# Kernel optimization log

Measured on AMD Instinct MI355X. Metric: run time of the kernel, lower is better.

## Reference

```python
import jax, jax.numpy as jnp
import numpy as np

N = 8192      # agent_num
F = 128       # feature dim
P = 16        # persona dim
E = 262144    # edges (N * avg_degree 32)


def setup_inputs() -> dict:
    key = jax.random.key(0)
    ks = jax.random.split(key, 10)
    return {
        "feature": jax.random.normal(ks[0], (N, F), dtype=jnp.float32),
        "next_feature": jax.random.normal(ks[1], (N, F), dtype=jnp.float32),
        "persona_t": jax.random.uniform(ks[2], (N, P), dtype=jnp.float32),
        "alpha": jax.random.normal(ks[3], (P,), dtype=jnp.float32),
        "beta": jax.random.normal(ks[4], (P,), dtype=jnp.float32),
        "gamma": jax.random.normal(ks[5], (P,), dtype=jnp.float32),
        "act_src": jax.random.randint(ks[6], (E,), 0, N, dtype=jnp.int32),
        "act_dst": jax.random.randint(ks[7], (E,), 0, N, dtype=jnp.int32),
        "edge_src": jax.random.randint(ks[8], (E,), 0, N, dtype=jnp.int32),
        "edge_dst": jax.random.randint(ks[9], (E,), 0, N, dtype=jnp.int32),
    }


def _row_l2_normalize(x):
    # norm_func: divide each row by its L2 norm (scatter-add of squares in torch)
    norms = jnp.sqrt(jnp.sum(x * x, axis=1, keepdims=True))
    return x / norms


def reference(feature, next_feature, persona_t, alpha, beta, gamma,
              act_src, act_dst, edge_src, edge_dst):
    n, f = feature.shape

    # ---- impact (gamma) path: adj_sim_self(next_action, old - new) ----
    diff = feature - next_feature                           # [N, F]
    # hadamard(adj, diff @ diff.T): only dot products on action edges
    impact_vals = jnp.sum(diff[act_src] * diff[act_dst], axis=1) / f   # [E]
    gamma_row = persona_t @ gamma                            # [N] persona-weighted gamma
    reward_impact = impact_vals * gamma_row[act_src]         # row-wise multiply

    # ---- similarity (alpha) path: adj_sim(next_action, norm(next_feature)) ----
    # step() normalizes next_feature, then adj_sim normalizes again (idempotent)
    nf = _row_l2_normalize(_row_l2_normalize(next_feature))  # [N, F]
    sim_vals = jnp.sum(nf[act_src] * nf[act_dst], axis=1)    # [E] cosine sims on edges
    alpha_row = persona_t @ alpha                            # [N]
    reward_sim = sim_vals * alpha_row[act_src]

    # ---- cost (beta) path: old edges (binary) * persona_beta broadcast over rows ----
    beta_row = persona_t @ beta                              # [N]
    reward_cost = beta_row[edge_src]                         # [E] (edge value = 1)

    # ---- reward = reward_sim - reward_cost + reward_impact on the union of supports ----
    reward = jnp.zeros((n, n), dtype=feature.dtype)
    reward = reward.at[act_src, act_dst].add(reward_sim + reward_impact)
    reward = reward.at[edge_src, edge_dst].add(-reward_cost)
    return reward
```

## Files before the change

kernel.cpp:

```cpp
#include <hip/hip_runtime.h>
#include <hip/hip_fp16.h>

#define N_AGENTS 8192
#define FDIM 128
#define PDIM 16
#define NEDGES 262144
#define CAP 128
#define OVERCAP 4096

typedef float floatx4 __attribute__((ext_vector_type(4)));
typedef int   intx2   __attribute__((ext_vector_type(2)));

__global__ __launch_bounds__(256) void row_prep_k(
        const float* __restrict__ feature,
        const float* __restrict__ next_feature,
        const float* __restrict__ persona,
        const float* __restrict__ alpha,
        const float* __restrict__ beta,
        const float* __restrict__ gamma,
        __half2* __restrict__ T2,
        float2* __restrict__ scale,
        float* __restrict__ brow,
        int* __restrict__ cnt,
        int* __restrict__ ocnt) {
    int row  = (blockIdx.x * blockDim.x + threadIdx.x) >> 6;
    int lane = threadIdx.x & 63;
    if (blockIdx.x == 0 && threadIdx.x == 0) *ocnt = 0;
    if (row >= N_AGENTS) return;

    const float2* f2 = (const float2*)(feature      + (size_t)row * FDIM);
    const float2* n2 = (const float2*)(next_feature + (size_t)row * FDIM);
    float2 f  = f2[lane];
    float2 nx = n2[lane];

    float2 d = make_float2(f.x - nx.x, f.y - nx.y);
    float ss = nx.x * nx.x + nx.y * nx.y;

    float pa = 0.f, pb = 0.f, pg = 0.f;
    if (lane < PDIM) {
        float p = persona[(size_t)row * PDIM + lane];
        pa = p * alpha[lane];
        pb = p * beta[lane];
        pg = p * gamma[lane];
    }

    #pragma unroll
    for (int off = 32; off > 0; off >>= 1) {
        ss += __shfl_xor(ss, off);
        pa += __shfl_xor(pa, off);
        pb += __shfl_xor(pb, off);
        pg += __shfl_xor(pg, off);
    }

    float inv = 1.0f / sqrtf(ss);
    __half2* trow = T2 + (size_t)row * 128;
    trow[lane]      = __float22half2_rn(make_float2(nx.x * inv, nx.y * inv));
    trow[64 + lane] = __float22half2_rn(d);

    if (lane == 0) {
        scale[row] = make_float2(pa, pg * (1.0f / FDIM));
        brow[row]  = pb;
        cnt[row]   = 0;
    }
}

__device__ inline float dot8(float4 a, float4 b) {
    const __half2* ha = (const __half2*)&a;
    const __half2* hb = (const __half2*)&b;
    float s = 0.f;
    #pragma unroll
    for (int j = 0; j < 4; ++j) {
        float2 fa = __half22float2(ha[j]);
        float2 fb = __half22float2(hb[j]);
        s += fa.x * fb.x + fa.y * fb.y;
    }
    return s;
}

__device__ inline void push_rec(int s, int d, float val,
                                int* cnt, intx2* bins,
                                int* ocnt, int4* olist) {
    int pos = atomicAdd(&cnt[s], 1);
    if (pos < CAP) {
        intx2 rec;
        rec.x = d;
        rec.y = __float_as_int(val);
        __builtin_nontemporal_store(rec, &bins[(size_t)s * CAP + pos]);
    } else {
        int op = atomicAdd(ocnt, 1);
        if (op < OVERCAP) olist[op] = make_int4(s, d, __float_as_int(val), 0);
    }
}

#define ACT_BLOCKS ((NEDGES * 16) / 256)
#define COST_BLOCKS (NEDGES / 256)
__global__ __launch_bounds__(256) void edge_bin_k(
        const int* __restrict__ asrc,
        const int* __restrict__ adst,
        const int* __restrict__ esrc,
        const int* __restrict__ edst,
        const __half* __restrict__ T,
        const float2* __restrict__ scale,
        const float* __restrict__ brow,
        int* __restrict__ cnt,
        intx2* __restrict__ bins,
        int* __restrict__ ocnt,
        int4* __restrict__ olist) {
    int b = blockIdx.x;
    if (b < ACT_BLOCKS) {
        int gid    = b * 256 + threadIdx.x;
        int e      = gid >> 4;
        int lane16 = gid & 15;
        int s = asrc[e];
        int d = adst[e];
        const float4* ts = (const float4*)(T + (size_t)s * 256);
        const float4* td = (const float4*)(T + (size_t)d * 256);
        int i0 = lane16 * 2;
        float acc = dot8(ts[i0], td[i0]) + dot8(ts[i0 + 1], td[i0 + 1]);
        acc += __shfl_xor(acc, 1, 16);
        acc += __shfl_xor(acc, 2, 16);
        acc += __shfl_xor(acc, 4, 16);
        float other = __shfl_xor(acc, 8, 16);
        if (lane16 == 0) {
            float2 sc = scale[s];
            float val = acc * sc.x + other * sc.y;
            push_rec(s, d, val, cnt, bins, ocnt, olist);
        }
    } else {
        int e = (b - ACT_BLOCKS) * 256 + threadIdx.x;
        int s = esrc[e];
        push_rec(s, edst[e], -brow[s], cnt, bins, ocnt, olist);
    }
}

__global__ __launch_bounds__(256) void row_assemble_k(
        const int* __restrict__ cnt,
        const intx2* __restrict__ bins,
        float* __restrict__ out) {
    __shared__ float rowbuf[N_AGENTS];
    int r   = blockIdx.x;
    int tid = threadIdx.x;

    floatx4* rb4 = (floatx4*)rowbuf;
    floatx4 z = (floatx4)0.f;
    #pragma unroll
    for (int i = 0; i < 8; ++i)
        rb4[tid + i * 256] = z;
    __syncthreads();

    int c = cnt[r];
    c = c < CAP ? c : CAP;
    for (int i = tid; i < c; i += 256) {
        intx2 rec = bins[(size_t)r * CAP + i];
        atomicAdd(&rowbuf[rec.x], __int_as_float(rec.y));
    }
    __syncthreads();

    floatx4* dst = (floatx4*)(out + (size_t)r * N_AGENTS);
    #pragma unroll
    for (int i = 0; i < 8; ++i)
        __builtin_nontemporal_store(rb4[tid + i * 256], &dst[tid + i * 256]);
}

__global__ __launch_bounds__(256) void overflow_k(
        const int* __restrict__ ocnt,
        const int4* __restrict__ olist,
        float* __restrict__ out) {
    int n = *ocnt;
    n = n < OVERCAP ? n : OVERCAP;
    for (int i = threadIdx.x; i < n; i += 256) {
        int4 rec = olist[i];
        atomicAdd(out + (size_t)rec.x * N_AGENTS + rec.y, __int_as_float(rec.z));
    }
}

extern "C" void kernel_launch(void* const* d_in, const int* in_sizes, int n_in,
                              void* d_out, int out_size, void* d_ws, size_t ws_size,
                              hipStream_t stream) {
    const float* feature      = (const float*)d_in[0];
    const float* next_feature = (const float*)d_in[1];
    const float* persona      = (const float*)d_in[2];
    const float* alpha        = (const float*)d_in[3];
    const float* beta         = (const float*)d_in[4];
    const float* gamma        = (const float*)d_in[5];
    const int*   act_src      = (const int*)d_in[6];
    const int*   act_dst      = (const int*)d_in[7];
    const int*   edge_src     = (const int*)d_in[8];
    const int*   edge_dst     = (const int*)d_in[9];

    float* out = (float*)d_out;

    char* ws = (char*)d_ws;
    __half* T     = (__half*)ws;                 ws += (size_t)N_AGENTS * 256 * sizeof(__half);
    float2* scale = (float2*)ws;                 ws += (size_t)N_AGENTS * sizeof(float2);
    float*  brow  = (float*)ws;                  ws += (size_t)N_AGENTS * sizeof(float);
    int*    cnt   = (int*)ws;                    ws += (size_t)N_AGENTS * sizeof(int);
    intx2*  bins  = (intx2*)ws;                  ws += (size_t)N_AGENTS * CAP * sizeof(intx2);
    int*    ocnt  = (int*)ws;                    ws += 16;
    int4*   olist = (int4*)ws;

    row_prep_k<<<N_AGENTS / 4, 256, 0, stream>>>(
        feature, next_feature, persona, alpha, beta, gamma,
        (__half2*)T, scale, brow, cnt, ocnt);

    edge_bin_k<<<ACT_BLOCKS + COST_BLOCKS, 256, 0, stream>>>(
        act_src, act_dst, edge_src, edge_dst,
        T, scale, brow, cnt, bins, ocnt, olist);

    row_assemble_k<<<N_AGENTS, 256, 0, stream>>>(cnt, bins, out);

    overflow_k<<<1, 256, 0, stream>>>(ocnt, olist, out);
}
```

Measured before the change: 336.7 us.

## Split row assembly into half-row bins and fold overflow into assembly

Each output row is binned into two half-rows keyed by destination column. The assembly kernel now uses a 16KB shared buffer per block over twice as many blocks, which should allow more resident blocks per CU for the write-bound zero-fill and store phase. The separate single-block overflow kernel is removed: every block scans the overflow list and applies the entries for its own half-row, saving a launch. Per-bin capacity drops to 96, so rows with more than 96 records in a half go to the overflow list. A large overflow list would then be scanned by all 16K blocks, and anything past the overflow cap is lost.

Measured after the change: 337.0 us. No clear change (+0.1%).

```diff
diff --git a/kernel.cpp b/kernel.cpp
--- a/kernel.cpp
+++ b/kernel.cpp
@@ -5,7 +5,9 @@
 #define FDIM 128
 #define PDIM 16
 #define NEDGES 262144
-#define CAP 128
+#define HALF 4096
+#define NBINS (N_AGENTS * 2)
+#define CAP 96
 #define OVERCAP 4096
 
 typedef float floatx4 __attribute__((ext_vector_type(4)));
@@ -60,7 +62,8 @@
     if (lane == 0) {
         scale[row] = make_float2(pa, pg * (1.0f / FDIM));
         brow[row]  = pb;
-        cnt[row]   = 0;
+        cnt[2 * row]     = 0;
+        cnt[2 * row + 1] = 0;
     }
 }
 
@@ -80,12 +83,13 @@
 __device__ inline void push_rec(int s, int d, float val,
                                 int* cnt, intx2* bins,
                                 int* ocnt, int4* olist) {
-    int pos = atomicAdd(&cnt[s], 1);
+    int hb = (s << 1) | (d >> 12);
+    int pos = atomicAdd(&cnt[hb], 1);
     if (pos < CAP) {
         intx2 rec;
-        rec.x = d;
+        rec.x = d & (HALF - 1);
         rec.y = __float_as_int(val);
-        __builtin_nontemporal_store(rec, &bins[(size_t)s * CAP + pos]);
+        __builtin_nontemporal_store(rec, &bins[(size_t)hb * CAP + pos]);
     } else {
         int op = atomicAdd(ocnt, 1);
         if (op < OVERCAP) olist[op] = make_int4(s, d, __float_as_int(val), 0);
@@ -133,45 +137,47 @@
     }
 }
 
-__global__ __launch_bounds__(256) void row_assemble_k(
+__global__ __launch_bounds__(256, 8) void row_assemble_k(
         const int* __restrict__ cnt,
         const intx2* __restrict__ bins,
-        float* __restrict__ out) {
-    __shared__ float rowbuf[N_AGENTS];
-    int r   = blockIdx.x;
-    int tid = threadIdx.x;
-
-    floatx4* rb4 = (floatx4*)rowbuf;
-    floatx4 z = (floatx4)0.f;
-    #pragma unroll
-    for (int i = 0; i < 8; ++i)
-        rb4[tid + i * 256] = z;
-    __syncthreads();
-
-    int c = cnt[r];
-    c = c < CAP ? c : CAP;
-    for (int i = tid; i < c; i += 256) {
-        intx2 rec = bins[(size_t)r * CAP + i];
-        atomicAdd(&rowbuf[rec.x], __int_as_float(rec.y));
-    }
-    __syncthreads();
-
-    floatx4* dst = (floatx4*)(out + (size_t)r * N_AGENTS);
-    #pragma unroll
-    for (int i = 0; i < 8; ++i)
-        __builtin_nontemporal_store(rb4[tid + i * 256], &dst[tid + i * 256]);
-}
-
-__global__ __launch_bounds__(256) void overflow_k(
         const int* __restrict__ ocnt,
         const int4* __restrict__ olist,
         float* __restrict__ out) {
+    __shared__ float rowbuf[HALF];
+    int hb  = blockIdx.x;
+    int r   = hb >> 1;
+    int h   = hb & 1;
+    int tid = threadIdx.x;
+
+    floatx4* rb4 = (floatx4*)rowbuf;
+    floatx4 z = (floatx4)0.f;
+    #pragma unroll
+    for (int i = 0; i < 4; ++i)
+        rb4[tid + i * 256] = z;
+    __syncthreads();
+
+    int c = cnt[hb];
+    c = c < CAP ? c : CAP;
+    if (tid < c) {
+        intx2 rec = bins[(size_t)hb * CAP + tid];
+        atomicAdd(&rowbuf[rec.x], __int_as_float(rec.y));
+    }
+
     int n = *ocnt;
-    n = n < OVERCAP ? n : OVERCAP;
-    for (int i = threadIdx.x; i < n; i += 256) {
-        int4 rec = olist[i];
-        atomicAdd(out + (size_t)rec.x * N_AGENTS + rec.y, __int_as_float(rec.z));
-    }
+    if (n > 0) {
+        n = n < OVERCAP ? n : OVERCAP;
+        for (int i = tid; i < n; i += 256) {
+            int4 rec = olist[i];
+            if (rec.x == r && (rec.y >> 12) == h)
+                atomicAdd(&rowbuf[rec.y & (HALF - 1)], __int_as_float(rec.z));
+        }
+    }
+    __syncthreads();
+
+    floatx4* dst = (floatx4*)(out + (size_t)r * N_AGENTS + (size_t)h * HALF);
+    #pragma unroll
+    for (int i = 0; i < 4; ++i)
+        __builtin_nontemporal_store(rb4[tid + i * 256], &dst[tid + i * 256]);
 }
 
 extern "C" void kernel_launch(void* const* d_in, const int* in_sizes, int n_in,
@@ -194,8 +200,8 @@
     __half* T     = (__half*)ws;                 ws += (size_t)N_AGENTS * 256 * sizeof(__half);
     float2* scale = (float2*)ws;                 ws += (size_t)N_AGENTS * sizeof(float2);
     float*  brow  = (float*)ws;                  ws += (size_t)N_AGENTS * sizeof(float);
-    int*    cnt   = (int*)ws;                    ws += (size_t)N_AGENTS * sizeof(int);
-    intx2*  bins  = (intx2*)ws;                  ws += (size_t)N_AGENTS * CAP * sizeof(intx2);
+    int*    cnt   = (int*)ws;                    ws += (size_t)NBINS * sizeof(int);
+    intx2*  bins  = (intx2*)ws;                  ws += (size_t)NBINS * CAP * sizeof(intx2);
     int*    ocnt  = (int*)ws;                    ws += 16;
     int4*   olist = (int4*)ws;
 
@@ -207,7 +213,5 @@
         act_src, act_dst, edge_src, edge_dst,
         T, scale, brow, cnt, bins, ocnt, olist);
 
-    row_assemble_k<<<N_AGENTS, 256, 0, stream>>>(cnt, bins, out);
-
-    overflow_k<<<1, 256, 0, stream>>>(ocnt, olist, out);
-}
+    row_assemble_k<<<NBINS, 256, 0, stream>>>(cnt, bins, ocnt, olist, out);
+}
```
